# Performance work log

Hardware: AMD Instinct MI355X
Metric: run time of the kernel (lower is better)

The kernel has to match this reference:

```python
import jax, jax.numpy as jnp
import numpy as np

B, L, DM = 16, 1024, 512
DI, ST, DC, RK, OD = 1024, 16, 4, 32, 128


def setup_inputs() -> dict:
    key = jax.random.key(0)
    ks = jax.random.split(key, 10)
    s = 0.02
    x = jax.random.normal(ks[0], (B, L, DM), dtype=jnp.float32)
    W_in = jax.random.normal(ks[1], (DM, 2 * DI), dtype=jnp.float32) * s
    conv_w = jax.random.normal(ks[2], (DI, DC), dtype=jnp.float32) * 0.2
    conv_b = jax.random.normal(ks[3], (DI,), dtype=jnp.float32) * s
    W_xproj = jax.random.normal(ks[4], (DI, RK + 2 * ST), dtype=jnp.float32) * s
    W_dt = jax.random.normal(ks[5], (RK, DI), dtype=jnp.float32) * s
    b_dt = jax.random.normal(ks[6], (DI,), dtype=jnp.float32) * s
    # S4D-real init: A_log[d, n] = log(n+1)
    A_log = jnp.log(jnp.tile(jnp.arange(1, ST + 1, dtype=jnp.float32)[None, :], (DI, 1)))
    Dp = jnp.ones((DI,), dtype=jnp.float32)
    W_out = jax.random.normal(ks[7], (DI, DM), dtype=jnp.float32) * s
    W_fc = jax.random.normal(ks[8], (L * DM, OD), dtype=jnp.float32) * 0.002
    b_fc = jnp.zeros((OD,), dtype=jnp.float32)
    return {"x": x, "W_in": W_in, "conv_w": conv_w, "conv_b": conv_b,
            "W_xproj": W_xproj, "W_dt": W_dt, "b_dt": b_dt, "A_log": A_log,
            "Dp": Dp, "W_out": W_out, "W_fc": W_fc, "b_fc": b_fc}


def _silu(v):
    return v * jax.nn.sigmoid(v)


def reference(x, W_in, conv_w, conv_b, W_xproj, W_dt, b_dt, A_log, Dp, W_out, W_fc, b_fc):
    b, l, dm = x.shape
    di, dc = conv_w.shape
    rk = W_dt.shape[0]
    st = A_log.shape[1]
    # in_proj -> split into x branch and gate z
    xz = x @ W_in                                # [B,L,2*DI]
    xin, z = jnp.split(xz, 2, axis=-1)
    # causal depthwise conv1d, kernel size dc, truncated to length l
    xp = jnp.pad(xin, ((0, 0), (dc - 1, 0), (0, 0)))
    conv = conv_b
    for j in range(dc):                          # fixed small kernel loop
        conv = conv + xp[:, j:j + l, :] * conv_w[:, j]
    xc = _silu(conv)                             # [B,L,DI]
    # input-dependent dt, B, C
    x_dbl = xc @ W_xproj                         # [B,L,RK+2*ST]
    dt = jax.nn.softplus(x_dbl[..., :rk] @ W_dt + b_dt)   # [B,L,DI]
    Bm = x_dbl[..., rk:rk + st]                  # [B,L,ST]
    Cm = x_dbl[..., rk + st:]                    # [B,L,ST]
    A = -jnp.exp(A_log)                          # [DI,ST]
    # selective scan: h_t = exp(dt_t*A)*h_{t-1} + dt_t*B_t*u_t ; y_t = C_t . h_t
    def step(h, inp):
        dt_t, B_t, C_t, u_t = inp                # [B,DI],[B,ST],[B,ST],[B,DI]
        dA = jnp.exp(dt_t[:, :, None] * A)       # [B,DI,ST]
        h = h * dA + (dt_t * u_t)[:, :, None] * B_t[:, None, :]
        y = jnp.einsum('bds,bs->bd', h, C_t)
        return h, y
    h0 = jnp.zeros((b, di, st), dtype=x.dtype)
    seq = (dt.transpose(1, 0, 2), Bm.transpose(1, 0, 2),
           Cm.transpose(1, 0, 2), xc.transpose(1, 0, 2))
    _, ys = jax.lax.scan(step, h0, seq)          # ys: [L,B,DI]
    y = ys.transpose(1, 0, 2) + Dp * xc          # skip connection
    y = y * _silu(z)                             # gate
    out = y @ W_out                              # [B,L,DM]
    # flatten + fc
    return out.reshape(b, -1) @ W_fc + b_fc      # [B,OD]
```

## Files before the change

### kernel.cpp

```cpp
#include <hip/hip_runtime.h>
#include <hip/hip_bf16.h>

typedef __hip_bfloat16 bf16;
typedef __bf16 bf8v __attribute__((ext_vector_type(8)));
typedef __bf16 bf4v __attribute__((ext_vector_type(4)));
typedef float f4v __attribute__((ext_vector_type(4)));

static __device__ __forceinline__ float tf(const bf16 v) { return __bfloat162float(v); }

static __device__ __forceinline__ float ldv(const void* p, size_t i, bool f32) {
    return f32 ? ((const float*)p)[i] : tf(((const bf16*)p)[i]);
}

static __device__ __forceinline__ void gld_lds16(const bf16* g, __bf16* l) {
    __builtin_amdgcn_global_load_lds(
        (const __attribute__((address_space(1))) void*)g,
        (__attribute__((address_space(3))) void*)l, 16, 0, 0);
}

constexpr int Bz = 16, Lz = 1024, DM = 512, DI = 1024, ST = 16, DC = 4, RK = 32, OD = 128;
constexpr int Mrows = Bz * Lz;
constexpr int XD = RK + 2 * ST;
constexpr int NC = 8, CT = Lz / NC;
constexpr int FC_KC = 512;
constexpr int FC_BLOCKS = (Lz * DM) / FC_KC;

__global__ void detect_kernel(const void* __restrict__ xp, int* __restrict__ flag) {
    int i = blockIdx.x * 256 + threadIdx.x;
    const bf16* p = (const bf16*)xp;
    float v = tf(p[(size_t)i * 64]);
    if (!(fabsf(v) < 1e4f)) atomicAdd(flag, 1);
}

__global__ __launch_bounds__(256) void canon_kernel(const void* __restrict__ src,
                                                    bf16* __restrict__ dst,
                                                    const int* __restrict__ flag) {
    const bool f = (*flag != 0);
    size_t base = ((size_t)blockIdx.x * 256 + threadIdx.x) * 8;
    if (!f) {
        *(uint4*)((__bf16*)dst + base) = *(const uint4*)((const bf16*)src + base);
    } else {
        f4v a = *(const f4v*)((const float*)src + base);
        f4v b = *(const f4v*)((const float*)src + base + 4);
        bf8v o;
        #pragma unroll
        for (int j = 0; j < 4; ++j) { o[j] = (__bf16)a[j]; o[j + 4] = (__bf16)b[j]; }
        *(bf8v*)((__bf16*)dst + base) = o;
    }
}

__global__ __launch_bounds__(256) void transpose3_kernel(const void* __restrict__ W0,
                                                         const void* __restrict__ W1,
                                                         const void* __restrict__ W2,
                                                         bf16* __restrict__ T0,
                                                         bf16* __restrict__ T1,
                                                         bf16* __restrict__ T2,
                                                         const int* __restrict__ flag) {
    const bool f = (*flag != 0);
    __shared__ float tile[32][33];
    int bid = blockIdx.x;
    const void* W; bf16* Wt; int K, N, n0, k0;
    if (bid < 1024) {
        W = W0; Wt = T0; K = DM; N = 2 * DI; n0 = (bid & 63) * 32; k0 = (bid >> 6) * 32;
    } else if (bid < 1536) {
        int b = bid - 1024;
        W = W1; Wt = T1; K = DI; N = DM; n0 = (b & 15) * 32; k0 = (b >> 4) * 32;
    } else {
        int b = bid - 1536;
        W = W2; Wt = T2; K = DI; N = XD; n0 = (b & 1) * 32; k0 = (b >> 1) * 32;
    }
    int c = threadIdx.x & 31, r4 = threadIdx.x >> 5;
    #pragma unroll
    for (int i = 0; i < 4; ++i) {
        int r = r4 + i * 8;
        tile[r][c] = ldv(W, (size_t)(k0 + r) * N + n0 + c, f);
    }
    __syncthreads();
    #pragma unroll
    for (int i = 0; i < 4; ++i) {
        int rr = r4 + i * 8;
        Wt[(size_t)(n0 + rr) * K + k0 + c] = __float2bfloat16(tile[c][rr]);
    }
}

template <int NT, bool SPLIT, bool CF32, int GXL>
__global__ __launch_bounds__(256) void gemm_bt(const bf16* __restrict__ A, int lda,
                                               const bf16* __restrict__ Bt, int ldb,
                                               void* __restrict__ C0, void* __restrict__ C1,
                                               int ldc, int K) {
    constexpr int MI = (NT == 128) ? 4 : 2;
    constexpr int NI = 4;
    constexpr int GX = 1 << GXL;
    __shared__ __align__(16) __bf16 As[2][128 * 32];
    __shared__ __align__(16) __bf16 Bs[2][NT * 32];
    const int tid = threadIdx.x, lane = tid & 63, w = tid >> 6;
    const int l15 = lane & 15, quad = lane >> 4;
    const int wm = (NT == 128) ? (w >> 1) * 64 : w * 32;
    const int wn = (NT == 128) ? (w & 1) * 64 : 0;

    const int nwg = GX * gridDim.y;
    const int bid = blockIdx.y * GX + blockIdx.x;
    const int swz = (bid & 7) * (nwg >> 3) + (bid >> 3);
    const int m0 = (swz >> GXL) * 128, n0 = (swz & (GX - 1)) * NT;

    f4v acc[MI][NI];
    #pragma unroll
    for (int i = 0; i < MI; ++i)
        #pragma unroll
        for (int j = 0; j < NI; ++j)
            #pragma unroll
            for (int r = 0; r < 4; ++r) acc[i][j][r] = 0.f;

    const int arow = w * 32 + (lane >> 2), ach = lane & 3;
    const int brow = w * 16 + (lane >> 2);

    auto stage = [&](int bi, int k0) {
        {
            const bf16* g0 = A + (size_t)(m0 + arow) * lda + k0 + ach * 8;
            gld_lds16(g0, &As[bi][w * 1024 + lane * 8]);
            gld_lds16(g0 + (size_t)16 * lda, &As[bi][w * 1024 + 512 + lane * 8]);
        }
        if constexpr (NT == 128) {
            const bf16* g0 = Bt + (size_t)(n0 + arow) * ldb + k0 + ach * 8;
            gld_lds16(g0, &Bs[bi][w * 1024 + lane * 8]);
            gld_lds16(g0 + (size_t)16 * ldb, &Bs[bi][w * 1024 + 512 + lane * 8]);
        } else {
            const bf16* g0 = Bt + (size_t)(n0 + brow) * ldb + k0 + ach * 8;
            gld_lds16(g0, &Bs[bi][w * 512 + lane * 8]);
        }
    };

    stage(0, 0);
    __syncthreads();
    int cur = 0;
    for (int k0 = 0; k0 < K; k0 += 32) {
        if (k0 + 32 < K) stage(cur ^ 1, k0 + 32);
        bf8v a[MI], b[NI];
        #pragma unroll
        for (int mi = 0; mi < MI; ++mi)
            a[mi] = *(const bf8v*)&As[cur][(wm + mi * 16 + l15) * 32 + quad * 8];
        #pragma unroll
        for (int ni = 0; ni < NI; ++ni)
            b[ni] = *(const bf8v*)&Bs[cur][(wn + ni * 16 + l15) * 32 + quad * 8];
        #pragma unroll
        for (int mi = 0; mi < MI; ++mi)
            #pragma unroll
            for (int ni = 0; ni < NI; ++ni)
                acc[mi][ni] = __builtin_amdgcn_mfma_f32_16x16x32_bf16(a[mi], b[ni], acc[mi][ni], 0, 0, 0);
        __syncthreads();
        cur ^= 1;
    }
    #pragma unroll
    for (int mi = 0; mi < MI; ++mi)
        #pragma unroll
        for (int ni = 0; ni < NI; ++ni)
            #pragma unroll
            for (int r = 0; r < 4; ++r) {
                int row = m0 + wm + mi * 16 + quad * 4 + r;
                int col = n0 + wn + ni * 16 + l15;
                float v = acc[mi][ni][r];
                if (SPLIT) {
                    if (col < DI) ((bf16*)C0)[(size_t)row * DI + col] = __float2bfloat16(v);
                    else ((bf16*)C1)[(size_t)row * DI + col - DI] =
                             __float2bfloat16(v / (1.f + __expf(-v)));
                } else if (CF32) {
                    ((float*)C0)[(size_t)row * ldc + col] = v;
                } else {
                    ((bf16*)C0)[(size_t)row * ldc + col] = __float2bfloat16(v);
                }
            }
}

__global__ __launch_bounds__(256) void conv_silu_kernel(const bf16* __restrict__ xin,
                                                        const void* __restrict__ conv_w,
                                                        const void* __restrict__ conv_b,
                                                        bf16* __restrict__ xc,
                                                        const int* __restrict__ flag) {
    const bool f = (*flag != 0);
    int g = blockIdx.x * 256 + threadIdx.x;
    int d = g & (DI - 1);
    int t = (g >> 10) & (Lz - 1);
    int b = g >> 20;
    const bf16* xin_b = xin + (size_t)b * Lz * DI;
    float acc = ldv(conv_b, d, f);
    #pragma unroll
    for (int j = 0; j < DC; ++j) {
        int tt = t + j - (DC - 1);
        if (tt >= 0) acc += tf(xin_b[(size_t)tt * DI + d]) * ldv(conv_w, d * DC + j, f);
    }
    xc[(size_t)g] = __float2bfloat16(acc / (1.f + __expf(-acc)));
}

__global__ __launch_bounds__(256) void dt_kernel(const float* __restrict__ x_dbl,
                                                 const void* __restrict__ W_dt,
                                                 const void* __restrict__ b_dt,
                                                 _Float16* __restrict__ dt,
                                                 const int* __restrict__ flag) {
    const bool f = (*flag != 0);
    int g = blockIdx.x * 256 + threadIdx.x;
    int d = g & (DI - 1);
    int m = g >> 10;
    float acc = ldv(b_dt, d, f);
    const float* xr = x_dbl + (size_t)m * XD;
    #pragma unroll
    for (int k = 0; k < RK; ++k) acc += xr[k] * ldv(W_dt, (size_t)k * DI + d, f);
    float dtv = (acc > 15.f) ? acc : __logf(1.f + __expf(acc));
    dt[(size_t)g] = (_Float16)dtv;
}

__global__ __launch_bounds__(256) void scan_pass1(const float* __restrict__ x_dbl,
                                                  const _Float16* __restrict__ dt,
                                                  const bf16* __restrict__ xc,
                                                  const void* __restrict__ A_log,
                                                  float* __restrict__ hbuf,
                                                  float* __restrict__ dtsum,
                                                  const int* __restrict__ flag) {
    const bool f = (*flag != 0);
    const int c = blockIdx.x, b = blockIdx.z;
    const int d = blockIdx.y * 256 + threadIdx.x;
    __shared__ float Brow[CT][16];
    #pragma unroll
    for (int i = 0; i < 2; ++i) {
        int idx = threadIdx.x + i * 256;
        int r = idx >> 2, q = idx & 3;
        *(f4v*)&Brow[r][q * 4] =
            *(const f4v*)(x_dbl + ((size_t)(b * Lz + c * CT + r)) * XD + RK + q * 4);
    }
    __syncthreads();
    float A[ST];
    #pragma unroll
    for (int s = 0; s < ST; ++s) A[s] = -__expf(ldv(A_log, (size_t)d * ST + s, f));
    float h[ST] = {};
    float S = 0.f;
    const _Float16* dtp = dt + (size_t)(b * Lz + c * CT) * DI + d;
    const bf16*     xcp = xc + (size_t)(b * Lz + c * CT) * DI + d;
    for (int t = 0; t < CT; ++t) {
        float dtv = (float)dtp[(size_t)t * DI];
        float du  = dtv * tf(xcp[(size_t)t * DI]);
        S += dtv;
        #pragma unroll
        for (int s = 0; s < ST; ++s)
            h[s] = h[s] * __expf(dtv * A[s]) + du * Brow[t][s];
    }
    float* hp = hbuf + ((size_t)(b * DI + d) * NC + c) * 16;
    #pragma unroll
    for (int s = 0; s < ST; ++s) hp[s] = h[s];
    dtsum[(size_t)(b * DI + d) * NC + c] = S;
}

__global__ __launch_bounds__(256) void scan_prefix(float* __restrict__ hbuf,
                                                   const float* __restrict__ dtsum,
                                                   const void* __restrict__ A_log,
                                                   const int* __restrict__ flag) {
    const bool f = (*flag != 0);
    int g2 = blockIdx.x * 256 + threadIdx.x;
    int d = g2 & (DI - 1);
    float A[ST];
    #pragma unroll
    for (int s = 0; s < ST; ++s) A[s] = -__expf(ldv(A_log, (size_t)d * ST + s, f));
    float hrun[ST] = {};
    for (int c = 0; c < NC; ++c) {
        float* hp = hbuf + ((size_t)g2 * NC + c) * 16;
        float S = dtsum[(size_t)g2 * NC + c];
        #pragma unroll
        for (int s = 0; s < ST; ++s) {
            float he = hp[s];
            float P = __expf(A[s] * S);
            hp[s] = hrun[s];
            hrun[s] = hrun[s] * P + he;
        }
    }
}

__global__ __launch_bounds__(256) void scan_pass2(const float* __restrict__ x_dbl,
                                                  const _Float16* __restrict__ dt,
                                                  const bf16* __restrict__ xc,
                                                  const void* __restrict__ A_log,
                                                  const void* __restrict__ Dp,
                                                  bf16* __restrict__ yzs,
                                                  const float* __restrict__ hbuf,
                                                  const int* __restrict__ flag) {
    const bool f = (*flag != 0);
    const int c = blockIdx.x, b = blockIdx.z;
    const int d = blockIdx.y * 256 + threadIdx.x;
    __shared__ float BC[CT][32];
    #pragma unroll
    for (int i = 0; i < 4; ++i) {
        int idx = threadIdx.x + i * 256;
        int r = idx >> 3, q = idx & 7;
        *(f4v*)&BC[r][q * 4] =
            *(const f4v*)(x_dbl + ((size_t)(b * Lz + c * CT + r)) * XD + RK + q * 4);
    }
    __syncthreads();
    float A[ST];
    #pragma unroll
    for (int s = 0; s < ST; ++s) A[s] = -__expf(ldv(A_log, (size_t)d * ST + s, f));
    float Dp_d = ldv(Dp, d, f);
    float h[ST];
    const float* hp = hbuf + ((size_t)(b * DI + d) * NC + c) * 16;
    #pragma unroll
    for (int s = 0; s < ST; ++s) h[s] = hp[s];
    const _Float16* dtp = dt + (size_t)(b * Lz + c * CT) * DI + d;
    const bf16*     xcp = xc + (size_t)(b * Lz + c * CT) * DI + d;
    bf16*           yzp = yzs + (size_t)(b * Lz + c * CT) * DI + d;
    for (int t = 0; t < CT; ++t) {
        float dtv = (float)dtp[(size_t)t * DI];
        float u   = tf(xcp[(size_t)t * DI]);
        float du  = dtv * u;
        float p = 0.f;
        #pragma unroll
        for (int s = 0; s < ST; ++s) {
            h[s] = h[s] * __expf(dtv * A[s]) + du * BC[t][s];
            p += h[s] * BC[t][16 + s];
        }
        float zz = tf(yzp[(size_t)t * DI]);
        yzp[(size_t)t * DI] = __float2bfloat16((p + Dp_d * u) * zz);
    }
}

__global__ __launch_bounds__(256) void fc_partial_kernel(const bf16* __restrict__ out_pre,
                                                         const void* __restrict__ W_fc,
                                                         float* __restrict__ part,
                                                         const int* __restrict__ flag) {
    const bool f = (*flag != 0);
    __shared__ __align__(16) float u_lds[FC_KC][16];
    const int tid = threadIdx.x;
    const int k0 = blockIdx.x * FC_KC;

    #pragma unroll
    for (int i = 0; i < 4; ++i) {
        int cid = tid + i * 256;
        int b = cid & 15, c8 = cid >> 4;
        bf8v v = *(const bf8v*)&out_pre[(size_t)b * (Lz * DM) + k0 + c8 * 8];
        #pragma unroll
        for (int j = 0; j < 8; ++j) u_lds[c8 * 8 + j][b] = (float)v[j];
    }
    __syncthreads();

    const int ng = tid & 31, kr = tid >> 5;
    f4v acc[16];
    #pragma unroll
    for (int b = 0; b < 16; ++b)
        #pragma unroll
        for (int c = 0; c < 4; ++c) acc[b][c] = 0.f;

    if (f) {
        const float* Wp = (const float*)W_fc + (size_t)(k0 + kr) * OD + ng * 4;
        #pragma unroll 4
        for (int kk = 0; kk < FC_KC; kk += 8) {
            f4v w4 = *(const f4v*)(Wp + (size_t)kk * OD);
            int kl = kk + kr;
            #pragma unroll
            for (int q = 0; q < 4; ++q) {
                f4v uq = *(const f4v*)&u_lds[kl][q * 4];
                #pragma unroll
                for (int c = 0; c < 4; ++c) acc[q * 4 + c] += uq[c] * w4;
            }
        }
    } else {
        const bf16* Wp = (const bf16*)W_fc + (size_t)(k0 + kr) * OD + ng * 4;
        #pragma unroll 4
        for (int kk = 0; kk < FC_KC; kk += 8) {
            bf4v wv = *(const bf4v*)(Wp + (size_t)kk * OD);
            f4v w4;
            #pragma unroll
            for (int c = 0; c < 4; ++c) w4[c] = (float)wv[c];
            int kl = kk + kr;
            #pragma unroll
            for (int q = 0; q < 4; ++q) {
                f4v uq = *(const f4v*)&u_lds[kl][q * 4];
                #pragma unroll
                for (int c = 0; c < 4; ++c) acc[q * 4 + c] += uq[c] * w4;
            }
        }
    }

    #pragma unroll
    for (int b = 0; b < 16; ++b)
        #pragma unroll
        for (int c = 0; c < 4; ++c) acc[b][c] += __shfl_down(acc[b][c], 32);
    __syncthreads();
    f4v* redv = (f4v*)&u_lds[0][0];
    const int w = tid >> 6, lane = tid & 63;
    if (lane < 32) {
        #pragma unroll
        for (int b = 0; b < 16; ++b) redv[(b * 4 + w) * 32 + lane] = acc[b];
    }
    __syncthreads();
    #pragma unroll
    for (int i = 0; i < 2; ++i) {
        int og = tid + i * 256;
        int b = og >> 5, ngo = og & 31;
        f4v s = {0.f, 0.f, 0.f, 0.f};
        #pragma unroll
        for (int w2 = 0; w2 < 4; ++w2) s += redv[(b * 4 + w2) * 32 + ngo];
        *(f4v*)&part[(size_t)blockIdx.x * (Bz * OD) + b * OD + ngo * 4] = s;
    }
}

__global__ __launch_bounds__(256) void fc_reduce_kernel(const float* __restrict__ part,
                                                        float* __restrict__ accb) {
    const int o = blockIdx.x * 256 + threadIdx.x;
    const int s0 = blockIdx.y * (FC_BLOCKS / 16);
    float s = 0.f;
    for (int p = s0; p < s0 + FC_BLOCKS / 16; ++p) s += part[(size_t)p * (Bz * OD) + o];
    atomicAdd(&accb[o], s);
}

__global__ void fc_final_kernel(const float* __restrict__ accbuf,
                                const void* __restrict__ b_fc, void* __restrict__ out,
                                const int* __restrict__ flag) {
    const bool f = (*flag != 0);
    int i = blockIdx.x * 256 + threadIdx.x;
    if (i < Bz * OD) {
        float v = accbuf[i] + ldv(b_fc, i & (OD - 1), f);
        if (f) ((float*)out)[i] = v;
        else   ((bf16*)out)[i]  = __float2bfloat16(v);
    }
}

extern "C" void kernel_launch(void* const* d_in, const int* in_sizes, int n_in,
                              void* d_out, int out_size, void* d_ws, size_t ws_size,
                              hipStream_t stream) {
    const void* x       = d_in[0];
    const void* W_in    = d_in[1];
    const void* conv_w  = d_in[2];
    const void* conv_b  = d_in[3];
    const void* W_xproj = d_in[4];
    const void* W_dt    = d_in[5];
    const void* b_dt    = d_in[6];
    const void* A_log   = d_in[7];
    const void* Dp      = d_in[8];
    const void* W_out   = d_in[9];
    const void* W_fc    = d_in[10];
    const void* b_fc    = d_in[11];

    char* ws = (char*)d_ws;
    bf16*     xin    = (bf16*)(ws);
    _Float16* dt     = (_Float16*)(ws);
    float*    part   = (float*)(ws);
    bf16*     yzs    = (bf16*)(ws + 33554432ull);
    bf16*     xc     = (bf16*)(ws + 67108864ull);
    float*    x_dbl  = (float*)(ws + 100663296ull);
    bf16*     xb     = (bf16*)(ws + 104857600ull);
    bf16*     outp   = (bf16*)(ws + 104857600ull);
    float*    hbuf   = (float*)(ws + 121634816ull);
    float*    dtsum  = (float*)(ws + 130023424ull);
    bf16*     Wt_in  = (bf16*)(ws + 130547712ull);
    bf16*     Wt_out = (bf16*)(ws + 132644864ull);
    bf16*     Wt_xp  = (bf16*)(ws + 133693440ull);
    float*    accb   = (float*)(ws + 133824512ull);
    int*      flag   = (int*)(ws + 133832704ull);

    dim3 blk(256);
    hipMemsetAsync(flag, 0, 4, stream);
    detect_kernel<<<256, blk, 0, stream>>>(x, flag);
    canon_kernel<<<(Mrows * DM) / 2048, blk, 0, stream>>>(x, xb, flag);
    transpose3_kernel<<<1600, blk, 0, stream>>>(W_in, W_out, W_xproj,
                                                Wt_in, Wt_out, Wt_xp, flag);
    hipLaunchKernelGGL((gemm_bt<128, true, false, 4>), dim3(2 * DI / 128, Mrows / 128), blk, 0, stream,
                       xb, DM, Wt_in, DM, xin, yzs, DI, DM);
    conv_silu_kernel<<<(Mrows * DI) / 256, blk, 0, stream>>>(xin, conv_w, conv_b, xc, flag);
    hipLaunchKernelGGL((gemm_bt<64, false, true, 0>), dim3(1, Mrows / 128), blk, 0, stream,
                       xc, DI, Wt_xp, DI, x_dbl, (void*)0, XD, DI);
    dt_kernel<<<(Mrows * DI) / 256, blk, 0, stream>>>(x_dbl, W_dt, b_dt, dt, flag);
    scan_pass1<<<dim3(NC, DI / 256, Bz), blk, 0, stream>>>(x_dbl, dt, xc, A_log, hbuf, dtsum, flag);
    scan_prefix<<<(Bz * DI) / 256, blk, 0, stream>>>(hbuf, dtsum, A_log, flag);
    scan_pass2<<<dim3(NC, DI / 256, Bz), blk, 0, stream>>>(x_dbl, dt, xc, A_log, Dp, yzs, hbuf, flag);
    hipLaunchKernelGGL((gemm_bt<128, false, false, 2>), dim3(DM / 128, Mrows / 128), blk, 0, stream,
                       yzs, DI, Wt_out, DI, outp, (void*)0, DM, DI);
    hipMemsetAsync(accb, 0, Bz * OD * sizeof(float), stream);
    fc_partial_kernel<<<FC_BLOCKS, blk, 0, stream>>>(outp, W_fc, part, flag);
    fc_reduce_kernel<<<dim3((Bz * OD) / 256, 16), blk, 0, stream>>>(part, accb);
    fc_final_kernel<<<(Bz * OD + 255) / 256, blk, 0, stream>>>(accb, b_fc, d_out, flag);
}
```

Baseline: 907.1 us.

## Fuse dt projection and softplus into both scan passes, double chunk count

Removes the standalone dt kernel and recomputes the rank-32 dt projection plus softplus inside scan_pass1 and scan_pass2 from the full x_dbl row staged in shared memory, with W_dt held in registers. This eliminates writing and twice reading a [B,L,DI] fp16 dt tensor, trading that memory traffic for duplicated arithmetic in both passes. The scan chunk count is also doubled to raise parallelism, shortening each block's serial loop, and the workspace layout is moved to make room for the larger hbuf and dtsum. The fused passes now carry more registers, which may reduce occupancy.

```diff
diff --git a/kernel.cpp b/kernel.cpp
--- a/kernel.cpp
+++ b/kernel.cpp
@@ -21,7 +21,7 @@
 constexpr int Bz = 16, Lz = 1024, DM = 512, DI = 1024, ST = 16, DC = 4, RK = 32, OD = 128;
 constexpr int Mrows = Bz * Lz;
 constexpr int XD = RK + 2 * ST;
-constexpr int NC = 8, CT = Lz / NC;
+constexpr int NC = 16, CT = Lz / NC;
 constexpr int FC_KC = 512;
 constexpr int FC_BLOCKS = (Lz * DM) / FC_KC;
 
@@ -191,56 +191,46 @@
     xc[(size_t)g] = __float2bfloat16(acc / (1.f + __expf(-acc)));
 }
 
-__global__ __launch_bounds__(256) void dt_kernel(const float* __restrict__ x_dbl,
-                                                 const void* __restrict__ W_dt,
-                                                 const void* __restrict__ b_dt,
-                                                 _Float16* __restrict__ dt,
-                                                 const int* __restrict__ flag) {
-    const bool f = (*flag != 0);
-    int g = blockIdx.x * 256 + threadIdx.x;
-    int d = g & (DI - 1);
-    int m = g >> 10;
-    float acc = ldv(b_dt, d, f);
-    const float* xr = x_dbl + (size_t)m * XD;
-    #pragma unroll
-    for (int k = 0; k < RK; ++k) acc += xr[k] * ldv(W_dt, (size_t)k * DI + d, f);
-    float dtv = (acc > 15.f) ? acc : __logf(1.f + __expf(acc));
-    dt[(size_t)g] = (_Float16)dtv;
-}
-
 __global__ __launch_bounds__(256) void scan_pass1(const float* __restrict__ x_dbl,
-                                                  const _Float16* __restrict__ dt,
                                                   const bf16* __restrict__ xc,
                                                   const void* __restrict__ A_log,
+                                                  const void* __restrict__ W_dt,
+                                                  const void* __restrict__ b_dt,
                                                   float* __restrict__ hbuf,
                                                   float* __restrict__ dtsum,
                                                   const int* __restrict__ flag) {
     const bool f = (*flag != 0);
     const int c = blockIdx.x, b = blockIdx.z;
     const int d = blockIdx.y * 256 + threadIdx.x;
-    __shared__ float Brow[CT][16];
-    #pragma unroll
-    for (int i = 0; i < 2; ++i) {
+    __shared__ float Row[CT][XD];
+    #pragma unroll
+    for (int i = 0; i < 4; ++i) {
         int idx = threadIdx.x + i * 256;
-        int r = idx >> 2, q = idx & 3;
-        *(f4v*)&Brow[r][q * 4] =
-            *(const f4v*)(x_dbl + ((size_t)(b * Lz + c * CT + r)) * XD + RK + q * 4);
-    }
-    __syncthreads();
+        int r = idx >> 4, q = idx & 15;
+        *(f4v*)&Row[r][q * 4] =
+            *(const f4v*)(x_dbl + ((size_t)(b * Lz + c * CT + r)) * XD + q * 4);
+    }
+    float W[RK];
+    #pragma unroll
+    for (int k = 0; k < RK; ++k) W[k] = ldv(W_dt, (size_t)k * DI + d, f);
+    const float bdt = ldv(b_dt, d, f);
     float A[ST];
     #pragma unroll
     for (int s = 0; s < ST; ++s) A[s] = -__expf(ldv(A_log, (size_t)d * ST + s, f));
+    __syncthreads();
     float h[ST] = {};
     float S = 0.f;
-    const _Float16* dtp = dt + (size_t)(b * Lz + c * CT) * DI + d;
-    const bf16*     xcp = xc + (size_t)(b * Lz + c * CT) * DI + d;
+    const bf16* xcp = xc + (size_t)(b * Lz + c * CT) * DI + d;
     for (int t = 0; t < CT; ++t) {
-        float dtv = (float)dtp[(size_t)t * DI];
+        float acc = bdt;
+        #pragma unroll
+        for (int k = 0; k < RK; ++k) acc += Row[t][k] * W[k];
+        float dtv = (acc > 15.f) ? acc : __logf(1.f + __expf(acc));
         float du  = dtv * tf(xcp[(size_t)t * DI]);
         S += dtv;
         #pragma unroll
         for (int s = 0; s < ST; ++s)
-            h[s] = h[s] * __expf(dtv * A[s]) + du * Brow[t][s];
+            h[s] = h[s] * __expf(dtv * A[s]) + du * Row[t][RK + s];
     }
     float* hp = hbuf + ((size_t)(b * DI + d) * NC + c) * 16;
     #pragma unroll
@@ -273,9 +263,10 @@
 }
 
 __global__ __launch_bounds__(256) void scan_pass2(const float* __restrict__ x_dbl,
-                                                  const _Float16* __restrict__ dt,
                                                   const bf16* __restrict__ xc,
                                                   const void* __restrict__ A_log,
+                                                  const void* __restrict__ W_dt,
+                                                  const void* __restrict__ b_dt,
                                                   const void* __restrict__ Dp,
                                                   bf16* __restrict__ yzs,
                                                   const float* __restrict__ hbuf,
@@ -283,35 +274,41 @@
     const bool f = (*flag != 0);
     const int c = blockIdx.x, b = blockIdx.z;
     const int d = blockIdx.y * 256 + threadIdx.x;
-    __shared__ float BC[CT][32];
+    __shared__ float Row[CT][XD];
     #pragma unroll
     for (int i = 0; i < 4; ++i) {
         int idx = threadIdx.x + i * 256;
-        int r = idx >> 3, q = idx & 7;
-        *(f4v*)&BC[r][q * 4] =
-            *(const f4v*)(x_dbl + ((size_t)(b * Lz + c * CT + r)) * XD + RK + q * 4);
-    }
-    __syncthreads();
+        int r = idx >> 4, q = idx & 15;
+        *(f4v*)&Row[r][q * 4] =
+            *(const f4v*)(x_dbl + ((size_t)(b * Lz + c * CT + r)) * XD + q * 4);
+    }
+    float W[RK];
+    #pragma unroll
+    for (int k = 0; k < RK; ++k) W[k] = ldv(W_dt, (size_t)k * DI + d, f);
+    const float bdt = ldv(b_dt, d, f);
     float A[ST];
     #pragma unroll
     for (int s = 0; s < ST; ++s) A[s] = -__expf(ldv(A_log, (size_t)d * ST + s, f));
     float Dp_d = ldv(Dp, d, f);
+    __syncthreads();
     float h[ST];
     const float* hp = hbuf + ((size_t)(b * DI + d) * NC + c) * 16;
     #pragma unroll
     for (int s = 0; s < ST; ++s) h[s] = hp[s];
-    const _Float16* dtp = dt + (size_t)(b * Lz + c * CT) * DI + d;
-    const bf16*     xcp = xc + (size_t)(b * Lz + c * CT) * DI + d;
-    bf16*           yzp = yzs + (size_t)(b * Lz + c * CT) * DI + d;
+    const bf16* xcp = xc + (size_t)(b * Lz + c * CT) * DI + d;
+    bf16*       yzp = yzs + (size_t)(b * Lz + c * CT) * DI + d;
     for (int t = 0; t < CT; ++t) {
-        float dtv = (float)dtp[(size_t)t * DI];
+        float acc = bdt;
+        #pragma unroll
+        for (int k = 0; k < RK; ++k) acc += Row[t][k] * W[k];
+        float dtv = (acc > 15.f) ? acc : __logf(1.f + __expf(acc));
         float u   = tf(xcp[(size_t)t * DI]);
         float du  = dtv * u;
         float p = 0.f;
         #pragma unroll
         for (int s = 0; s < ST; ++s) {
-            h[s] = h[s] * __expf(dtv * A[s]) + du * BC[t][s];
-            p += h[s] * BC[t][16 + s];
+            h[s] = h[s] * __expf(dtv * A[s]) + du * Row[t][RK + s];
+            p += h[s] * Row[t][RK + ST + s];
         }
         float zz = tf(yzp[(size_t)t * DI]);
         yzp[(size_t)t * DI] = __float2bfloat16((p + Dp_d * u) * zz);
@@ -437,20 +434,19 @@
 
     char* ws = (char*)d_ws;
     bf16*     xin    = (bf16*)(ws);
-    _Float16* dt     = (_Float16*)(ws);
     float*    part   = (float*)(ws);
     bf16*     yzs    = (bf16*)(ws + 33554432ull);
     bf16*     xc     = (bf16*)(ws + 67108864ull);
     float*    x_dbl  = (float*)(ws + 100663296ull);
     bf16*     xb     = (bf16*)(ws + 104857600ull);
     bf16*     outp   = (bf16*)(ws + 104857600ull);
-    float*    hbuf   = (float*)(ws + 121634816ull);
-    float*    dtsum  = (float*)(ws + 130023424ull);
-    bf16*     Wt_in  = (bf16*)(ws + 130547712ull);
-    bf16*     Wt_out = (bf16*)(ws + 132644864ull);
-    bf16*     Wt_xp  = (bf16*)(ws + 133693440ull);
-    float*    accb   = (float*)(ws + 133824512ull);
-    int*      flag   = (int*)(ws + 133832704ull);
+    float*    hbuf   = (float*)(ws + 167772160ull);
+    float*    dtsum  = (float*)(ws + 188743680ull);
+    bf16*     Wt_in  = (bf16*)(ws + 199229440ull);
+    bf16*     Wt_out = (bf16*)(ws + 202375168ull);
+    bf16*     Wt_xp  = (bf16*)(ws + 204472320ull);
+    float*    accb   = (float*)(ws + 205520896ull);
+    int*      flag   = (int*)(ws + 206569472ull);
 
     dim3 blk(256);
     hipMemsetAsync(flag, 0, 4, stream);
@@ -463,10 +459,11 @@
     conv_silu_kernel<<<(Mrows * DI) / 256, blk, 0, stream>>>(xin, conv_w, conv_b, xc, flag);
     hipLaunchKernelGGL((gemm_bt<64, false, true, 0>), dim3(1, Mrows / 128), blk, 0, stream,
                        xc, DI, Wt_xp, DI, x_dbl, (void*)0, XD, DI);
-    dt_kernel<<<(Mrows * DI) / 256, blk, 0, stream>>>(x_dbl, W_dt, b_dt, dt, flag);
-    scan_pass1<<<dim3(NC, DI / 256, Bz), blk, 0, stream>>>(x_dbl, dt, xc, A_log, hbuf, dtsum, flag);
+    scan_pass1<<<dim3(NC, DI / 256, Bz), blk, 0, stream>>>(x_dbl, xc, A_log, W_dt, b_dt,
+                                                           hbuf, dtsum, flag);
     scan_prefix<<<(Bz * DI) / 256, blk, 0, stream>>>(hbuf, dtsum, A_log, flag);
-    scan_pass2<<<dim3(NC, DI / 256, Bz), blk, 0, stream>>>(x_dbl, dt, xc, A_log, Dp, yzs, hbuf, flag);
+    scan_pass2<<<dim3(NC, DI / 256, Bz), blk, 0, stream>>>(x_dbl, xc, A_log, W_dt, b_dt,
+                                                           Dp, yzs, hbuf, flag);
     hipLaunchKernelGGL((gemm_bt<128, false, false, 2>), dim3(DM / 128, Mrows / 128), blk, 0, stream,
                        yzs, DI, Wt_out, DI, outp, (void*)0, DM, DI);
     hipMemsetAsync(accb, 0, Bz * OD * sizeof(float), stream);
```

Result: faster. 790.1 us (-12.9%).
